# Optimization experiments

Hardware: AMD Instinct MI355X
Metric: run time of the kernel (lower is better)

## Reference

```python
import jax, jax.numpy as jnp
import numpy as np

SEQ_LEN = 4096
EMBED_DIM = 2048
NUM_HEADS = 16
HEAD_DIM = EMBED_DIM // NUM_HEADS


def setup_inputs() -> dict:
    key = jax.random.key(0)
    k1, k2, k3 = jax.random.split(key, 3)
    x = jax.random.normal(k1, (SEQ_LEN, EMBED_DIM), dtype=jnp.float32)
    # Dense-layer params (lecun-normal-ish scaling for stability)
    W_qkv = jax.random.normal(k2, (EMBED_DIM, 3 * EMBED_DIM), dtype=jnp.float32) / np.sqrt(EMBED_DIM)
    b_qkv = jnp.zeros((3 * EMBED_DIM,), dtype=jnp.float32)
    W_out = jax.random.normal(k3, (EMBED_DIM, EMBED_DIM), dtype=jnp.float32) / np.sqrt(EMBED_DIM)
    b_out = jnp.zeros((EMBED_DIM,), dtype=jnp.float32)
    return {"x": x, "W_qkv": W_qkv, "b_qkv": b_qkv, "W_out": W_out, "b_out": b_out}


def reference(x, W_qkv, b_qkv, W_out, b_out):
    seq_len = x.shape[0]
    qkv = x @ W_qkv + b_qkv                       # (S, 3E)
    qkv = qkv.reshape(seq_len, 3, NUM_HEADS, HEAD_DIM)
    q, k, v = qkv[:, 0], qkv[:, 1], qkv[:, 2]     # each (S, H, D)
    scale = 1.0 / jnp.sqrt(jnp.float32(HEAD_DIM))
    # NOTE: faithful to source -- contracts over BOTH heads and head_dim,
    # producing a single (S, S) attention matrix shared across heads.
    attn = jnp.einsum('thd,shd->ts', q, k) * scale
    causal = jnp.triu(jnp.ones((seq_len, seq_len), dtype=bool), k=1)
    attn = jnp.where(causal, -jnp.inf, attn)
    attn = jax.nn.softmax(attn, axis=-1)
    out = jnp.einsum('ts,shd->thd', attn, v)      # (S, H, D)
    out = out.reshape(seq_len, EMBED_DIM)
    return out @ W_out + b_out
```

## Files before the change

kernel.cpp:

```cpp
#include <hip/hip_runtime.h>
#include <cstdint>
#include <cstddef>

#define SEQLEN 4096
#define EMBED  2048
#define NH     16
#define HD     128
#define N3     6144
#define SCALE  0.08838834764831845f
#define MBIAS  25.0f
#define LB4    12288
#define LB2    8192

typedef __attribute__((ext_vector_type(8))) short bf16x8;
typedef __attribute__((ext_vector_type(4))) float f32x4;
typedef unsigned short u16;

#define MFMA(a, b, c) __builtin_amdgcn_mfma_f32_16x16x32_bf16((a), (b), (c), 0, 0, 0)

__device__ inline u16 f2bf(float f) {
  uint32_t u = __float_as_uint(f);
  u += 0x7FFF + ((u >> 16) & 1);
  return (u16)(u >> 16);
}

__device__ inline float bf2f(u16 u) {
  return __uint_as_float(((uint32_t)u) << 16);
}

__device__ inline void gload_lds16(const u16* g, u16* l) {
  __builtin_amdgcn_global_load_lds((const __attribute__((address_space(1))) void*)g,
                                   (__attribute__((address_space(3))) void*)l, 16, 0, 0);
}

__device__ __forceinline__ void stage6(const u16* a0, const u16* a1, const u16* a2, const u16* a3,
                                       const u16* b0, const u16* b1, u16* base, int w, int lane) {
  gload_lds16(a0, base + w * 512 + lane * 8);
  gload_lds16(a1, base + 2048 + w * 512 + lane * 8);
  gload_lds16(a2, base + 4096 + w * 512 + lane * 8);
  gload_lds16(a3, base + 6144 + w * 512 + lane * 8);
  gload_lds16(b0, base + 8192 + w * 512 + lane * 8);
  gload_lds16(b1, base + 10240 + w * 512 + lane * 8);
}

__device__ __forceinline__ void mm256x128w4(const u16* gA, size_t sA, const u16* gB, size_t sB,
                                            int NT, u16* lds, f32x4 (&acc)[8][4]) {
  int tid = threadIdx.x;
  int w = tid >> 6, lane = tid & 63;
  int g = lane >> 4, lr = lane & 15;
  int wm = w >> 1, wn = w & 1;
  int arow = (w << 4) + (lane >> 2);
  int cb = (((lane & 3) ^ (arow & 3)) << 3);
  const u16* a0 = gA + (size_t)arow * sA + cb;
  const u16* a1 = a0 + (size_t)64 * sA;
  const u16* a2 = a0 + (size_t)128 * sA;
  const u16* a3 = a0 + (size_t)192 * sA;
  const u16* b0 = gB + (size_t)arow * sB + cb;
  const u16* b1 = b0 + (size_t)64 * sB;
  int gx = ((g ^ (lr & 3)) << 3);
  int aoff = ((wm << 7) + lr) * 32 + gx;
  int boff = 8192 + ((wn << 6) + lr) * 32 + gx;
  stage6(a0, a1, a2, a3, b0, b1, lds, w, lane);
  stage6(a0 + 32, a1 + 32, a2 + 32, a3 + 32, b0 + 32, b1 + 32, lds + LB4, w, lane);
  asm volatile("s_waitcnt vmcnt(6)" ::: "memory");
  __builtin_amdgcn_s_barrier();
  for (int t = 0; t < NT; ++t) {
    u16* base = lds + (t % 3) * LB4;
    bf16x8 af[8], bfr[4];
    #pragma unroll
    for (int m = 0; m < 8; m++) af[m] = *(const bf16x8*)(base + aoff + m * 512);
    #pragma unroll
    for (int n = 0; n < 4; n++) bfr[n] = *(const bf16x8*)(base + boff + n * 512);
    if (t + 2 < NT) {
      int kt = (t + 2) << 5;
      stage6(a0 + kt, a1 + kt, a2 + kt, a3 + kt, b0 + kt, b1 + kt,
             lds + ((t + 2) % 3) * LB4, w, lane);
    }
    __builtin_amdgcn_s_setprio(1);
    #pragma unroll
    for (int m = 0; m < 8; m++)
      #pragma unroll
      for (int n = 0; n < 4; n++)
        acc[m][n] = MFMA(af[m], bfr[n], acc[m][n]);
    __builtin_amdgcn_s_setprio(0);
    if (t + 1 < NT) {
      if (t + 2 < NT) asm volatile("s_waitcnt vmcnt(6)" ::: "memory");
      else            asm volatile("s_waitcnt vmcnt(0)" ::: "memory");
      __builtin_amdgcn_s_barrier();
    }
  }
  asm volatile("" ::: "memory");
}

__device__ __forceinline__ void stage4h(const u16* a0, const u16* a1, const u16* b0, const u16* b1,
                                        u16* base, int w, int lane) {
  gload_lds16(a0, base + w * 512 + lane * 8);
  gload_lds16(a1, base + 2048 + w * 512 + lane * 8);
  gload_lds16(b0, base + 4096 + w * 512 + lane * 8);
  gload_lds16(b1, base + 6144 + w * 512 + lane * 8);
}

__device__ __forceinline__ void mm128x128w4(const u16* gA, size_t sA, const u16* gB, size_t sB,
                                            int NT, u16* lds, f32x4 (&acc)[4][4]) {
  int tid = threadIdx.x;
  int w = tid >> 6, lane = tid & 63;
  int g = lane >> 4, lr = lane & 15;
  int wm = w >> 1, wn = w & 1;
  int arow = (w << 4) + (lane >> 2);
  int cb = (((lane & 3) ^ (arow & 3)) << 3);
  const u16* a0 = gA + (size_t)arow * sA + cb;
  const u16* a1 = a0 + (size_t)64 * sA;
  const u16* b0 = gB + (size_t)arow * sB + cb;
  const u16* b1 = b0 + (size_t)64 * sB;
  int gx = ((g ^ (lr & 3)) << 3);
  int aoff = wm * 2048 + lr * 32 + gx;
  int boff = 4096 + wn * 2048 + lr * 32 + gx;
  stage4h(a0, a1, b0, b1, lds, w, lane);
  stage4h(a0 + 32, a1 + 32, b0 + 32, b1 + 32, lds + LB2, w, lane);
  asm volatile("s_waitcnt vmcnt(4)" ::: "memory");
  __builtin_amdgcn_s_barrier();
  for (int t = 0; t < NT; ++t) {
    u16* base = lds + (t % 3) * LB2;
    bf16x8 af[4], bfr[4];
    #pragma unroll
    for (int m = 0; m < 4; m++) af[m] = *(const bf16x8*)(base + aoff + m * 512);
    #pragma unroll
    for (int n = 0; n < 4; n++) bfr[n] = *(const bf16x8*)(base + boff + n * 512);
    if (t + 2 < NT) {
      int kt = (t + 2) << 5;
      stage4h(a0 + kt, a1 + kt, b0 + kt, b1 + kt, lds + ((t + 2) % 3) * LB2, w, lane);
    }
    __builtin_amdgcn_s_setprio(1);
    #pragma unroll
    for (int m = 0; m < 4; m++)
      #pragma unroll
      for (int n = 0; n < 4; n++)
        acc[m][n] = MFMA(af[m], bfr[n], acc[m][n]);
    __builtin_amdgcn_s_setprio(0);
    if (t + 1 < NT) {
      if (t + 2 < NT) asm volatile("s_waitcnt vmcnt(4)" ::: "memory");
      else            asm volatile("s_waitcnt vmcnt(0)" ::: "memory");
      __builtin_amdgcn_s_barrier();
    }
  }
  asm volatile("" ::: "memory");
}

__global__ __launch_bounds__(256) void conv_f32_bf16(const float* __restrict__ in,
                                                     u16* __restrict__ out, int n) {
  int i = (blockIdx.x * 256 + threadIdx.x) * 4;
  if (i >= n) return;
  float4 v = *(const float4*)(in + i);
  ushort4 o;
  o.x = f2bf(v.x); o.y = f2bf(v.y); o.z = f2bf(v.z); o.w = f2bf(v.w);
  *(ushort4*)(out + i) = o;
}

__global__ __launch_bounds__(256) void transpose_conv(const float* __restrict__ in,
                                                      u16* __restrict__ out, int R, int C) {
  __shared__ float t[32][33];
  int c0 = blockIdx.x * 32, r0 = blockIdx.y * 32;
  int tx = threadIdx.x, ty = threadIdx.y;
  #pragma unroll
  for (int i = ty; i < 32; i += 8)
    t[i][tx] = in[(size_t)(r0 + i) * C + c0 + tx];
  __syncthreads();
  #pragma unroll
  for (int i = ty; i < 32; i += 8)
    out[(size_t)(c0 + i) * R + r0 + tx] = f2bf(t[tx][i]);
}

__global__ __launch_bounds__(256) void vtrans(const u16* __restrict__ qkv, u16* __restrict__ vT) {
  __shared__ u16 t[32][33];
  int c0 = blockIdx.x * 32, t0 = blockIdx.y * 32;
  int tx = threadIdx.x, ty = threadIdx.y;
  #pragma unroll
  for (int i = ty; i < 32; i += 8)
    t[i][tx] = qkv[(size_t)(t0 + i) * N3 + 2 * EMBED + c0 + tx];
  __syncthreads();
  #pragma unroll
  for (int i = ty; i < 32; i += 8)
    vT[(size_t)(c0 + i) * SEQLEN + t0 + tx] = t[tx][i];
}

__global__ __launch_bounds__(256, 2) void gemm_bt4(const u16* __restrict__ A, const u16* __restrict__ Bt,
                                                   const float* __restrict__ bias,
                                                   u16* __restrict__ Cb, int N, int K) {
  __shared__ __align__(16) u16 lds[3 * LB4];
  int bm = blockIdx.x, bn = blockIdx.y;
  f32x4 acc[8][4] = {};
  mm256x128w4(A + (size_t)(bm * 256) * K, K, Bt + (size_t)(bn * 128) * K, K, K >> 5, lds, acc);
  int tid = threadIdx.x;
  int w = tid >> 6, lane = tid & 63, g = lane >> 4, lr = lane & 15;
  int wm = w >> 1, wn = w & 1;
  int r0 = bm * 256 + wm * 128, c0 = bn * 128 + wn * 64;
  #pragma unroll
  for (int n = 0; n < 4; n++) {
    int c = c0 + n * 16 + lr;
    float bv = bias[c];
    #pragma unroll
    for (int m = 0; m < 8; m++)
      #pragma unroll
      for (int j = 0; j < 4; j++) {
        int r = r0 + m * 16 + g * 4 + j;
        Cb[(size_t)r * N + c] = f2bf(acc[m][n][j] + bv);
      }
  }
}

__global__ __launch_bounds__(256, 2) void gemm_bt4f(const u16* __restrict__ A, const u16* __restrict__ Bt,
                                                    const float* __restrict__ bias,
                                                    float* __restrict__ Cf, int N, int K) {
  __shared__ __align__(16) u16 lds[3 * LB4];
  int bm = blockIdx.x, bn = blockIdx.y;
  f32x4 acc[8][4] = {};
  mm256x128w4(A + (size_t)(bm * 256) * K, K, Bt + (size_t)(bn * 128) * K, K, K >> 5, lds, acc);
  int tid = threadIdx.x;
  int w = tid >> 6, lane = tid & 63, g = lane >> 4, lr = lane & 15;
  int wm = w >> 1, wn = w & 1;
  int r0 = bm * 256 + wm * 128, c0 = bn * 128 + wn * 64;
  #pragma unroll
  for (int n = 0; n < 4; n++) {
    int c = c0 + n * 16 + lr;
    float bv = bias[c];
    #pragma unroll
    for (int m = 0; m < 8; m++)
      #pragma unroll
      for (int j = 0; j < 4; j++) {
        int r = r0 + m * 16 + g * 4 + j;
        Cf[(size_t)r * N + c] = acc[m][n][j] + bv;
      }
  }
}

__global__ __launch_bounds__(256, 2) void sgemm_p4(const u16* __restrict__ qkv,
                                                   u16* __restrict__ P,
                                                   float* __restrict__ Lpart) {
  int by = blockIdx.x, bx = blockIdx.y;
  int r0g = by * 256, c0g = bx * 128;
  if (c0g > r0g + 255) return;
  __shared__ __align__(16) u16 lds[3 * LB4];
  f32x4 acc[8][4] = {};
  mm256x128w4(qkv + (size_t)r0g * N3, N3, qkv + (size_t)c0g * N3 + EMBED, N3, EMBED >> 5, lds, acc);
  int tid = threadIdx.x;
  int w = tid >> 6, lane = tid & 63, g = lane >> 4, lr = lane & 15;
  int wm = w >> 1, wn = w & 1;
  int r0 = r0g + wm * 128, c0 = c0g + wn * 64;
  int slot = bx * 2 + wn;
  #pragma unroll
  for (int m = 0; m < 8; m++)
    #pragma unroll
    for (int j = 0; j < 4; j++) {
      int r = r0 + m * 16 + g * 4 + j;
      float psv = 0.f;
      #pragma unroll
      for (int n = 0; n < 4; n++) {
        int c = c0 + n * 16 + lr;
        float p = (c <= r) ? __expf(fmaf(acc[m][n][j], SCALE, -MBIAS)) : 0.f;
        P[(size_t)r * SEQLEN + c] = f2bf(p);
        psv += p;
      }
      psv += __shfl_xor(psv, 1);  psv += __shfl_xor(psv, 2);
      psv += __shfl_xor(psv, 4);  psv += __shfl_xor(psv, 8);
      if (lr == 0) Lpart[(size_t)r * 64 + slot] = psv;
    }
}

__global__ __launch_bounds__(256) void psum_small(const float* __restrict__ Lpart,
                                                  float* __restrict__ L) {
  int wave = threadIdx.x >> 6, lane = threadIdx.x & 63;
  int r = blockIdx.x * 4 + wave;
  float s = Lpart[(size_t)r * 64 + lane];
  s += __shfl_xor(s, 1);  s += __shfl_xor(s, 2);  s += __shfl_xor(s, 4);
  s += __shfl_xor(s, 8);  s += __shfl_xor(s, 16); s += __shfl_xor(s, 32);
  if (lane == 0) L[r] = s;
}

__global__ __launch_bounds__(256, 2) void pv_gemm4(const u16* __restrict__ P,
                                                   const u16* __restrict__ vT,
                                                   const float* __restrict__ L,
                                                   u16* __restrict__ O) {
  __shared__ __align__(16) u16 lds[3 * LB2];
  int pp = blockIdx.x, bx = blockIdx.y;
  int tid = threadIdx.x;
  int w = tid >> 6, lane = tid & 63, g = lane >> 4, lr = lane & 15;
  int wm = w >> 1, wn = w & 1;
  int c0g = bx * 128;
  #pragma unroll
  for (int pass = 0; pass < 2; pass++) {
    int rt = pass ? pp : (31 - pp);
    int r0g = rt * 128;
    int NT = (r0g + 128) >> 5;
    f32x4 acc[4][4] = {};
    mm128x128w4(P + (size_t)r0g * SEQLEN, SEQLEN, vT + (size_t)c0g * SEQLEN, SEQLEN, NT, lds, acc);
    int r0 = r0g + wm * 64, c0 = c0g + wn * 64;
    #pragma unroll
    for (int m = 0; m < 4; m++) {
      float invl[4];
      #pragma unroll
      for (int j = 0; j < 4; j++)
        invl[j] = 1.f / L[r0 + m * 16 + g * 4 + j];
      #pragma unroll
      for (int n = 0; n < 4; n++) {
        int c = c0 + n * 16 + lr;
        #pragma unroll
        for (int j = 0; j < 4; j++) {
          int r = r0 + m * 16 + g * 4 + j;
          O[(size_t)r * EMBED + c] = f2bf(acc[m][n][j] * invl[j]);
        }
      }
    }
    __syncthreads();
  }
}

extern "C" void kernel_launch(void* const* d_in, const int* in_sizes, int n_in,
                              void* d_out, int out_size, void* d_ws, size_t ws_size,
                              hipStream_t stream) {
  const float* x     = (const float*)d_in[0];
  const float* W_qkv = (const float*)d_in[1];
  const float* b_qkv = (const float*)d_in[2];
  const float* W_out = (const float*)d_in[3];
  const float* b_out = (const float*)d_in[4];
  float* out = (float*)d_out;

  u16* xb    = (u16*)d_ws;
  u16* qkvb  = xb + (size_t)SEQLEN * EMBED;
  u16* Pbuf  = qkvb + (size_t)SEQLEN * N3;
  u16* vT    = Pbuf + (size_t)SEQLEN * SEQLEN;
  float* Lbuf = (float*)(vT + (size_t)EMBED * SEQLEN);
  u16* attb  = xb;
  u16* WqkvT = Pbuf;
  u16* WoutT = Pbuf;
  float* Lpart = (float*)xb;

  conv_f32_bf16<<<SEQLEN * EMBED / 1024, 256, 0, stream>>>(x, xb, SEQLEN * EMBED);
  transpose_conv<<<dim3(N3 / 32, EMBED / 32), dim3(32, 8), 0, stream>>>(W_qkv, WqkvT, EMBED, N3);
  gemm_bt4<<<dim3(SEQLEN / 256, N3 / 128), 256, 0, stream>>>(xb, WqkvT, b_qkv, qkvb, N3, EMBED);
  vtrans<<<dim3(EMBED / 32, SEQLEN / 32), dim3(32, 8), 0, stream>>>(qkvb, vT);
  hipMemsetAsync(Lpart, 0, (size_t)SEQLEN * 64 * sizeof(float), stream);
  sgemm_p4<<<dim3(SEQLEN / 256, SEQLEN / 128), 256, 0, stream>>>(qkvb, Pbuf, Lpart);
  psum_small<<<SEQLEN / 4, 256, 0, stream>>>(Lpart, Lbuf);
  pv_gemm4<<<dim3(16, EMBED / 128), 256, 0, stream>>>(Pbuf, vT, Lbuf, attb);
  transpose_conv<<<dim3(EMBED / 32, EMBED / 32), dim3(32, 8), 0, stream>>>(W_out, WoutT, EMBED, EMBED);
  gemm_bt4f<<<dim3(SEQLEN / 256, EMBED / 128), 256, 0, stream>>>(attb, WoutT, b_out, out, EMBED, EMBED);
}
```

Before: 321.7 us.

## Use 256x256 eight-wave pipelined GEMM for QKV and score kernels

Adds a new 512-thread GEMM mainloop (mm8p) over 256x256 tiles. It uses 128KB of dynamic LDS split into eight swizzled segments, and each phase issues its loads, waits on vmcnt, hits a barrier and runs MFMAs at raised wave priority. The QKV projection and the QK^T score kernel now use it. The score kernel launches only its 136 lower-triangular tiles, decoded from a linear block index, so early-exit blocks are no longer launched. The goal is more data reuse per tile and better overlap of loads with compute. The cost is fewer blocks, which may underfill the device in the 136-block score kernel, plus heavy LDS use that limits occupancy.

```diff
diff --git a/kernel.cpp b/kernel.cpp
--- a/kernel.cpp
+++ b/kernel.cpp
@@ -11,6 +11,7 @@
 #define MBIAS  25.0f
 #define LB4    12288
 #define LB2    8192
+#define LBP    8192
 
 typedef __attribute__((ext_vector_type(8))) short bf16x8;
 typedef __attribute__((ext_vector_type(4))) float f32x4;
@@ -31,6 +32,78 @@
 __device__ inline void gload_lds16(const u16* g, u16* l) {
   __builtin_amdgcn_global_load_lds((const __attribute__((address_space(1))) void*)g,
                                    (__attribute__((address_space(3))) void*)l, 16, 0, 0);
+}
+
+__device__ __forceinline__ void stage_seg(const u16* gX, size_t sX, int ktile, int h,
+                                          u16* seg, int tid) {
+  int row = tid >> 2, slotL = tid & 3;
+  int xorb = ((slotL ^ (row & 3)) << 3);
+  const u16* src = gX + (size_t)row * sX + ktile * 64 + h * 32 + xorb;
+  gload_lds16(src, seg + row * 32 + slotL * 8);
+  gload_lds16(src + (size_t)128 * sX, seg + (row + 128) * 32 + slotL * 8);
+}
+
+template<int P, int KK, int MH>
+__device__ __forceinline__ void phase8(u16* lds, int arow_off, int brow_off,
+                                       bf16x8 (&bfr)[4], f32x4 (&acc)[8][4],
+                                       const u16* sg, size_t ss, int stile, int sh,
+                                       u16* sseg, bool doStage, int tid) {
+  u16* segA = lds + (P * 4 + KK) * LBP;
+  u16* segB = lds + (P * 4 + 2 + KK) * LBP;
+  bf16x8 af[4];
+  #pragma unroll
+  for (int mi = 0; mi < 4; mi++)
+    af[mi] = *(const bf16x8*)(segA + arow_off + (MH * 4 + mi) * 512);
+  if (MH == 0) {
+    #pragma unroll
+    for (int n = 0; n < 4; n++)
+      bfr[n] = *(const bf16x8*)(segB + brow_off + n * 512);
+  }
+  if (doStage) stage_seg(sg, ss, stile, sh, sseg, tid);
+  asm volatile("s_waitcnt vmcnt(6)" ::: "memory");
+  __builtin_amdgcn_s_barrier();
+  __builtin_amdgcn_s_setprio(1);
+  #pragma unroll
+  for (int mi = 0; mi < 4; mi++)
+    #pragma unroll
+    for (int n = 0; n < 4; n++)
+      acc[MH * 4 + mi][n] = MFMA(af[mi], bfr[n], acc[MH * 4 + mi][n]);
+  __builtin_amdgcn_s_setprio(0);
+  __builtin_amdgcn_s_barrier();
+}
+
+__device__ __forceinline__ void mm8p(const u16* gA, size_t sA, const u16* gB, size_t sB,
+                                     int NTILES, u16* lds, f32x4 (&acc)[8][4]) {
+  int tid = threadIdx.x;
+  int lane = tid & 63, w = tid >> 6;
+  int g = lane >> 4, lr = lane & 15;
+  int wm = w >> 2, wn = w & 3;
+  int gx = (g ^ (lr & 3)) << 3;
+  int arow_off = (wm * 128 + lr) * 32 + gx;
+  int brow_off = (wn * 64 + lr) * 32 + gx;
+  stage_seg(gA, sA, 0, 0, lds + 0 * LBP, tid);
+  stage_seg(gB, sB, 0, 0, lds + 2 * LBP, tid);
+  stage_seg(gA, sA, 0, 1, lds + 1 * LBP, tid);
+  stage_seg(gB, sB, 0, 1, lds + 3 * LBP, tid);
+  stage_seg(gA, sA, 1, 0, lds + 4 * LBP, tid);
+  stage_seg(gB, sB, 1, 0, lds + 6 * LBP, tid);
+  asm volatile("s_waitcnt vmcnt(8)" ::: "memory");
+  __builtin_amdgcn_s_barrier();
+  int NI = NTILES >> 1;
+  for (int i = 0; i < NI; ++i) {
+    bool more = (i + 1 < NI);
+    int t2 = 2 * i + 2, t3 = 2 * i + 3;
+    bf16x8 bfr[4];
+    phase8<0,0,0>(lds, arow_off, brow_off, bfr, acc, gA, sA, 2*i+1, 1, lds + 5*LBP, true, tid);
+    phase8<0,0,1>(lds, arow_off, brow_off, bfr, acc, gB, sB, 2*i+1, 1, lds + 7*LBP, true, tid);
+    phase8<0,1,0>(lds, arow_off, brow_off, bfr, acc, gA, sA, t2, 0, lds + 0*LBP, more, tid);
+    phase8<0,1,1>(lds, arow_off, brow_off, bfr, acc, gB, sB, t2, 0, lds + 2*LBP, more, tid);
+    phase8<1,0,0>(lds, arow_off, brow_off, bfr, acc, gA, sA, t2, 1, lds + 1*LBP, more, tid);
+    phase8<1,0,1>(lds, arow_off, brow_off, bfr, acc, gB, sB, t2, 1, lds + 3*LBP, more, tid);
+    phase8<1,1,0>(lds, arow_off, brow_off, bfr, acc, gA, sA, t3, 0, lds + 4*LBP, more, tid);
+    phase8<1,1,1>(lds, arow_off, brow_off, bfr, acc, gB, sB, t3, 0, lds + 6*LBP, more, tid);
+  }
+  asm volatile("" ::: "memory");
 }
 
 __device__ __forceinline__ void stage6(const u16* a0, const u16* a1, const u16* a2, const u16* a3,
@@ -183,17 +256,17 @@
     vT[(size_t)(c0 + i) * SEQLEN + t0 + tx] = t[tx][i];
 }
 
-__global__ __launch_bounds__(256, 2) void gemm_bt4(const u16* __restrict__ A, const u16* __restrict__ Bt,
-                                                   const float* __restrict__ bias,
-                                                   u16* __restrict__ Cb, int N, int K) {
-  __shared__ __align__(16) u16 lds[3 * LB4];
+__global__ __launch_bounds__(512, 2) void gemm_qkv8p(const u16* __restrict__ A, const u16* __restrict__ Bt,
+                                                     const float* __restrict__ bias,
+                                                     u16* __restrict__ Cb, int N, int K) {
+  extern __shared__ __align__(16) u16 lds[];
   int bm = blockIdx.x, bn = blockIdx.y;
   f32x4 acc[8][4] = {};
-  mm256x128w4(A + (size_t)(bm * 256) * K, K, Bt + (size_t)(bn * 128) * K, K, K >> 5, lds, acc);
+  mm8p(A + (size_t)(bm * 256) * K, K, Bt + (size_t)(bn * 256) * K, K, K >> 6, lds, acc);
   int tid = threadIdx.x;
   int w = tid >> 6, lane = tid & 63, g = lane >> 4, lr = lane & 15;
-  int wm = w >> 1, wn = w & 1;
-  int r0 = bm * 256 + wm * 128, c0 = bn * 128 + wn * 64;
+  int wm = w >> 2, wn = w & 3;
+  int r0 = bm * 256 + wm * 128, c0 = bn * 256 + wn * 64;
   #pragma unroll
   for (int n = 0; n < 4; n++) {
     int c = c0 + n * 16 + lr;
@@ -208,45 +281,23 @@
   }
 }
 
-__global__ __launch_bounds__(256, 2) void gemm_bt4f(const u16* __restrict__ A, const u16* __restrict__ Bt,
-                                                    const float* __restrict__ bias,
-                                                    float* __restrict__ Cf, int N, int K) {
-  __shared__ __align__(16) u16 lds[3 * LB4];
-  int bm = blockIdx.x, bn = blockIdx.y;
-  f32x4 acc[8][4] = {};
-  mm256x128w4(A + (size_t)(bm * 256) * K, K, Bt + (size_t)(bn * 128) * K, K, K >> 5, lds, acc);
-  int tid = threadIdx.x;
-  int w = tid >> 6, lane = tid & 63, g = lane >> 4, lr = lane & 15;
-  int wm = w >> 1, wn = w & 1;
-  int r0 = bm * 256 + wm * 128, c0 = bn * 128 + wn * 64;
-  #pragma unroll
-  for (int n = 0; n < 4; n++) {
-    int c = c0 + n * 16 + lr;
-    float bv = bias[c];
-    #pragma unroll
-    for (int m = 0; m < 8; m++)
-      #pragma unroll
-      for (int j = 0; j < 4; j++) {
-        int r = r0 + m * 16 + g * 4 + j;
-        Cf[(size_t)r * N + c] = acc[m][n][j] + bv;
-      }
-  }
-}
-
-__global__ __launch_bounds__(256, 2) void sgemm_p4(const u16* __restrict__ qkv,
+__global__ __launch_bounds__(512, 2) void sgemm_p8(const u16* __restrict__ qkv,
                                                    u16* __restrict__ P,
                                                    float* __restrict__ Lpart) {
-  int by = blockIdx.x, bx = blockIdx.y;
-  int r0g = by * 256, c0g = bx * 128;
-  if (c0g > r0g + 255) return;
-  __shared__ __align__(16) u16 lds[3 * LB4];
+  extern __shared__ __align__(16) u16 lds[];
+  int idx = blockIdx.x;
+  int by = (int)((sqrtf(8.f * idx + 1.f) - 1.f) * 0.5f);
+  while ((by + 1) * (by + 2) / 2 <= idx) by++;
+  while (by * (by + 1) / 2 > idx) by--;
+  int bx = idx - by * (by + 1) / 2;
+  int r0g = by * 256, c0g = bx * 256;
   f32x4 acc[8][4] = {};
-  mm256x128w4(qkv + (size_t)r0g * N3, N3, qkv + (size_t)c0g * N3 + EMBED, N3, EMBED >> 5, lds, acc);
+  mm8p(qkv + (size_t)r0g * N3, N3, qkv + (size_t)c0g * N3 + EMBED, N3, EMBED >> 6, lds, acc);
   int tid = threadIdx.x;
   int w = tid >> 6, lane = tid & 63, g = lane >> 4, lr = lane & 15;
-  int wm = w >> 1, wn = w & 1;
+  int wm = w >> 2, wn = w & 3;
   int r0 = r0g + wm * 128, c0 = c0g + wn * 64;
-  int slot = bx * 2 + wn;
+  int slot = bx * 4 + wn;
   #pragma unroll
   for (int m = 0; m < 8; m++)
     #pragma unroll
@@ -266,6 +317,31 @@
     }
 }
 
+__global__ __launch_bounds__(256, 2) void gemm_bt4f(const u16* __restrict__ A, const u16* __restrict__ Bt,
+                                                    const float* __restrict__ bias,
+                                                    float* __restrict__ Cf, int N, int K) {
+  __shared__ __align__(16) u16 lds[3 * LB4];
+  int bm = blockIdx.x, bn = blockIdx.y;
+  f32x4 acc[8][4] = {};
+  mm256x128w4(A + (size_t)(bm * 256) * K, K, Bt + (size_t)(bn * 128) * K, K, K >> 5, lds, acc);
+  int tid = threadIdx.x;
+  int w = tid >> 6, lane = tid & 63, g = lane >> 4, lr = lane & 15;
+  int wm = w >> 1, wn = w & 1;
+  int r0 = bm * 256 + wm * 128, c0 = bn * 128 + wn * 64;
+  #pragma unroll
+  for (int n = 0; n < 4; n++) {
+    int c = c0 + n * 16 + lr;
+    float bv = bias[c];
+    #pragma unroll
+    for (int m = 0; m < 8; m++)
+      #pragma unroll
+      for (int j = 0; j < 4; j++) {
+        int r = r0 + m * 16 + g * 4 + j;
+        Cf[(size_t)r * N + c] = acc[m][n][j] + bv;
+      }
+  }
+}
+
 __global__ __launch_bounds__(256) void psum_small(const float* __restrict__ Lpart,
                                                   float* __restrict__ L) {
   int wave = threadIdx.x >> 6, lane = threadIdx.x & 63;
@@ -334,12 +410,16 @@
   u16* WoutT = Pbuf;
   float* Lpart = (float*)xb;
 
+  hipFuncSetAttribute((const void*)gemm_qkv8p, hipFuncAttributeMaxDynamicSharedMemorySize, 131072);
+  hipFuncSetAttribute((const void*)sgemm_p8,  hipFuncAttributeMaxDynamicSharedMemorySize, 131072);
+
   conv_f32_bf16<<<SEQLEN * EMBED / 1024, 256, 0, stream>>>(x, xb, SEQLEN * EMBED);
   transpose_conv<<<dim3(N3 / 32, EMBED / 32), dim3(32, 8), 0, stream>>>(W_qkv, WqkvT, EMBED, N3);
-  gemm_bt4<<<dim3(SEQLEN / 256, N3 / 128), 256, 0, stream>>>(xb, WqkvT, b_qkv, qkvb, N3, EMBED);
+  gemm_qkv8p<<<dim3(SEQLEN / 256, N3 / 256), 512, 131072, stream>>>(xb, WqkvT, b_qkv, qkvb,
+                                                                    N3, EMBED);
   vtrans<<<dim3(EMBED / 32, SEQLEN / 32), dim3(32, 8), 0, stream>>>(qkvb, vT);
   hipMemsetAsync(Lpart, 0, (size_t)SEQLEN * 64 * sizeof(float), stream);
-  sgemm_p4<<<dim3(SEQLEN / 256, SEQLEN / 128), 256, 0, stream>>>(qkvb, Pbuf, Lpart);
+  sgemm_p8<<<136, 512, 131072, stream>>>(qkvb, Pbuf, Lpart);
   psum_small<<<SEQLEN / 4, 256, 0, stream>>>(Lpart, Lbuf);
   pv_gemm4<<<dim3(16, EMBED / 128), 256, 0, stream>>>(Pbuf, vT, Lbuf, attb);
   transpose_conv<<<dim3(EMBED / 32, EMBED / 32), dim3(32, 8), 0, stream>>>(W_out, WoutT, EMBED, EMBED);
```

Measured after the change: 330.7 us. 1.03x slower.
